# Performance work log

Hardware: AMD Instinct MI355X
Metric: run time of the kernel (lower is better)

Reference implementation:

```python
import jax, jax.numpy as jnp
import numpy as np

N_NODES = 100000
N_EDGES = 1600000
HIDDEN = 128
STEPS = 4
N_GRAPHS = 64


def setup_inputs() -> dict:
    key = jax.random.key(0)
    ks = jax.random.split(key, 8)
    x = jax.random.normal(ks[0], (N_NODES, HIDDEN), dtype=jnp.float32)
    edge_index = jax.random.randint(ks[1], (2, N_EDGES), 0, N_NODES, dtype=jnp.int64)
    batch = jnp.sort(jax.random.randint(ks[2], (N_NODES,), 0, N_GRAPHS, dtype=jnp.int64))
    s = 1.0 / np.sqrt(HIDDEN)
    weight = jax.random.normal(ks[3], (STEPS, HIDDEN, HIDDEN), dtype=jnp.float32) * s
    w_ih = jax.random.normal(ks[4], (3 * HIDDEN, HIDDEN), dtype=jnp.float32) * s
    w_hh = jax.random.normal(ks[5], (3 * HIDDEN, HIDDEN), dtype=jnp.float32) * s
    b_ih = jnp.zeros((3 * HIDDEN,), dtype=jnp.float32)
    b_hh = jnp.zeros((3 * HIDDEN,), dtype=jnp.float32)
    return {"x": x, "edge_index": edge_index, "batch": batch,
            "weight": weight, "w_ih": w_ih, "w_hh": w_hh,
            "b_ih": b_ih, "b_hh": b_hh}


def _gru_cell(m, h, w_ih, w_hh, b_ih, b_hh):
    # PyTorch GRUCell: gates ordered (r, z, n)
    gi = m @ w_ih.T + b_ih  # [N, 3H]
    gh = h @ w_hh.T + b_hh  # [N, 3H]
    i_r, i_z, i_n = jnp.split(gi, 3, axis=-1)
    h_r, h_z, h_n = jnp.split(gh, 3, axis=-1)
    r = jax.nn.sigmoid(i_r + h_r)
    z = jax.nn.sigmoid(i_z + h_z)
    n = jnp.tanh(i_n + r * h_n)
    return (1.0 - z) * n + z * h


def reference(x, edge_index, batch, weight, w_ih, w_hh, b_ih, b_hh):
    src, dst = edge_index[0], edge_index[1]
    h = x
    for i in range(STEPS):
        m = h @ weight[i]  # [N, H]
        # message = m[src] scattered (add) into dst
        aggr = jax.ops.segment_sum(m[src], dst, num_segments=N_NODES)
        h = _gru_cell(aggr, h, w_ih, w_hh, b_ih, b_hh)
    h = jax.nn.relu(h)
    # global mean pool per graph
    sums = jax.ops.segment_sum(h, batch, num_segments=N_GRAPHS)  # [G, H]
    counts = jax.ops.segment_sum(jnp.ones((N_NODES,), h.dtype), batch, num_segments=N_GRAPHS)
    return sums / jnp.maximum(counts, 1.0)[:, None]
```

## Files before the change

### kernel.cpp

```cpp
#include <hip/hip_runtime.h>

#define N_NODES  100000
#define N_EDGES  1600000
#define HIDDEN   128
#define STEPS    4
#define N_GRAPHS 64
#define NBUCK    256
#define BWID     391
#define BCAP     7168

typedef unsigned short u16;
typedef unsigned int   u32;
typedef unsigned long long u64;
typedef __attribute__((ext_vector_type(8))) short bf16x8;
typedef __attribute__((ext_vector_type(4))) float f32x4;
typedef __attribute__((ext_vector_type(2))) float f32x2;

__device__ inline u16 f2bf(float f) {
  u32 u = __float_as_uint(f);
  u = (u + 0x7FFFu + ((u >> 16) & 1u)) >> 16;
  return (u16)u;
}
__device__ inline float bf2f(u16 b) { return __uint_as_float(((u32)b) << 16); }

__device__ inline float rcp_f(float x) { return __builtin_amdgcn_rcpf(x); }
__device__ inline float sig_f(float x) { return rcp_f(1.f + __expf(-x)); }
__device__ inline float tanh_f(float x) { return 1.f - 2.f * rcp_f(1.f + __expf(2.f * x)); }

__global__ __launch_bounds__(1024) void k_part(const int* __restrict__ esrc,
                                               const int* __restrict__ edst,
                                               int* __restrict__ gcursor,
                                               u32* __restrict__ ebuf) {
  __shared__ int hist[NBUCK];
  __shared__ int base[NBUCK];
  int tid = threadIdx.x;
  if (tid < NBUCK) hist[tid] = 0;
  __syncthreads();
  int e0 = blockIdx.x * 4096;
  int sv[4], dv[4], bk[4], rk[4];
  #pragma unroll
  for (int i = 0; i < 4; ++i) {
    int e = e0 + i * 1024 + tid;
    if (e < N_EDGES) {
      sv[i] = esrc[e];
      dv[i] = edst[e];
      bk[i] = (int)((u32)dv[i] / (u32)BWID);
      rk[i] = atomicAdd(&hist[bk[i]], 1);
    } else bk[i] = -1;
  }
  __syncthreads();
  if (tid < NBUCK) base[tid] = atomicAdd(&gcursor[tid], hist[tid]);
  __syncthreads();
  #pragma unroll
  for (int i = 0; i < 4; ++i) {
    if (bk[i] >= 0) {
      int pos = bk[i] * BCAP + base[bk[i]] + rk[i];
      ebuf[pos] = ((u32)(dv[i] - bk[i] * BWID) << 17) | (u32)sv[i];
    }
  }
}

__global__ void k_bscan(const int* __restrict__ gcursor, int* __restrict__ ebase) {
  __shared__ int buf[NBUCK];
  int t = threadIdx.x;
  int v = gcursor[t];
  buf[t] = v;
  __syncthreads();
  for (int off = 1; off < NBUCK; off <<= 1) {
    int u = 0;
    if (t >= off) u = buf[t - off];
    __syncthreads();
    buf[t] += u;
    __syncthreads();
  }
  ebase[t] = buf[t] - v;
  if (t == NBUCK - 1) ebase[NBUCK] = buf[t];
}

__global__ __launch_bounds__(1024) void k_csr(const u32* __restrict__ ebuf,
                                              const int* __restrict__ ebase,
                                              int* __restrict__ offs,
                                              int* __restrict__ csr) {
  __shared__ int lcnt[512];
  __shared__ int lofs[512];
  int b = blockIdx.x, tid = threadIdx.x;
  int n0 = b * BWID;
  int n1 = min(n0 + BWID, N_NODES);
  int nn = n1 - n0;
  int e0 = ebase[b];
  int cnt = ebase[b + 1] - e0;
  const u32* ebase_p = ebuf + (size_t)b * BCAP;
  if (tid < 512) lcnt[tid] = 0;
  __syncthreads();
  for (int e = tid; e < cnt; e += 1024) {
    int dst = (int)(ebase_p[e] >> 17);
    atomicAdd(&lcnt[dst], 1);
  }
  __syncthreads();
  if (tid < 512) lofs[tid] = lcnt[tid];
  __syncthreads();
  for (int off = 1; off < 512; off <<= 1) {
    int v = 0;
    if (tid < 512 && tid >= off) v = lofs[tid - off];
    __syncthreads();
    if (tid < 512 && tid >= off) lofs[tid] += v;
    __syncthreads();
  }
  int nodeoff = 0;
  if (tid < 512) nodeoff = e0 + lofs[tid] - lcnt[tid];
  if (tid < 512) lofs[tid] = nodeoff;
  if (tid < nn) offs[n0 + tid] = nodeoff;
  if (b == 0 && tid == 0) offs[N_NODES] = N_EDGES;
  __syncthreads();
  for (int e = tid; e < cnt; e += 1024) {
    u32 p = ebase_p[e];
    int src = (int)(p & 0x1FFFFu);
    int dst = (int)(p >> 17);
    int pos = atomicAdd(&lofs[dst], 1);
    csr[pos] = src;
  }
}

__global__ void k_wb(const float* __restrict__ W, const float* __restrict__ w_ih,
                     const float* __restrict__ w_hh, u16* __restrict__ bsw) {
  __shared__ float wrow[128];
  int b = blockIdx.x, st = b >> 8, k = b & 255, t = threadIdx.x;
  if (k < 128) wrow[t] = W[(st * 128 + k) * 128 + t];
  __syncthreads();
  int kc = k >> 5, quad = (k >> 3) & 3, kl = k & 7;
  u16* base = bsw + (size_t)st * 131072 + kc * 16384;
  #pragma unroll
  for (int gq = 0; gq < 4; ++gq) {
    int c = gq * 128 + t;
    float v;
    if (k < 128) {
      if (c < 384) {
        const float* wr = w_ih + c * 128;
        float sacc = 0.f;
        for (int j = 0; j < 128; ++j) sacc += wrow[j] * wr[j];
        v = sacc;
      } else v = 0.f;
    } else {
      int kk = k - 128;
      if (c < 256)      v = w_hh[c * 128 + kk];
      else if (c < 384) v = 0.f;
      else              v = w_hh[(c - 128) * 128 + kk];
    }
    int gi = c >> 7, cw = c & 127;
    int wv = cw >> 5, hu = (cw >> 4) & 1, nl = c & 15;
    int slot = wv * 8 + gi * 2 + hu;
    base[(slot * 4 + quad) * 128 + nl * 8 + kl] = f2bf(v);
  }
}

__global__ void k_convert(const float* __restrict__ x, u16* __restrict__ h) {
  int i = (blockIdx.x * 256 + threadIdx.x) * 4;
  float4 v = *(const float4*)(x + i);
  u16 o[4] = {f2bf(v.x), f2bf(v.y), f2bf(v.z), f2bf(v.w)};
  *(uint2*)(h + i) = *(uint2*)o;
}

__device__ inline void acc8(f32x2* a, uint4 p) {
  f32x2 v;
  v.x = __uint_as_float(p.x << 16); v.y = __uint_as_float(p.x & 0xffff0000u);
  a[0] += v;
  v.x = __uint_as_float(p.y << 16); v.y = __uint_as_float(p.y & 0xffff0000u);
  a[1] += v;
  v.x = __uint_as_float(p.z << 16); v.y = __uint_as_float(p.z & 0xffff0000u);
  a[2] += v;
  v.x = __uint_as_float(p.w << 16); v.y = __uint_as_float(p.w & 0xffff0000u);
  a[3] += v;
}

__global__ void k_gather(const u16* __restrict__ h, const int* __restrict__ csr,
                         const int* __restrict__ offs, u16* __restrict__ s) {
  int node = blockIdx.x * 4 + (threadIdx.x >> 6);
  int lane = threadIdx.x & 63;
  int q   = lane >> 4;
  int sub = lane & 15;
  int beg = offs[node], end = offs[node + 1];
  f32x2 a[4];
  a[0] = a[1] = a[2] = a[3] = (f32x2){0.f, 0.f};
  int j = beg + q;
  for (; j + 12 < end; j += 16) {
    int s0 = csr[j], s1 = csr[j + 4], s2 = csr[j + 8], s3 = csr[j + 12];
    uint4 p0 = *(const uint4*)(h + (size_t)s0 * 128 + sub * 8);
    uint4 p1 = *(const uint4*)(h + (size_t)s1 * 128 + sub * 8);
    uint4 p2 = *(const uint4*)(h + (size_t)s2 * 128 + sub * 8);
    uint4 p3 = *(const uint4*)(h + (size_t)s3 * 128 + sub * 8);
    acc8(a, p0); acc8(a, p1); acc8(a, p2); acc8(a, p3);
  }
  {
    int j0 = j, j1 = j + 4, j2 = j + 8, j3 = j + 12;
    u32 m0 = (j0 < end) ? 0xffffffffu : 0u;
    u32 m1 = (j1 < end) ? 0xffffffffu : 0u;
    u32 m2 = (j2 < end) ? 0xffffffffu : 0u;
    u32 m3 = (j3 < end) ? 0xffffffffu : 0u;
    int t0 = (j0 < end) ? j0 : 0, t1 = (j1 < end) ? j1 : 0;
    int t2 = (j2 < end) ? j2 : 0, t3 = (j3 < end) ? j3 : 0;
    int s0 = csr[t0], s1 = csr[t1], s2 = csr[t2], s3 = csr[t3];
    uint4 p0 = *(const uint4*)(h + (size_t)s0 * 128 + sub * 8);
    uint4 p1 = *(const uint4*)(h + (size_t)s1 * 128 + sub * 8);
    uint4 p2 = *(const uint4*)(h + (size_t)s2 * 128 + sub * 8);
    uint4 p3 = *(const uint4*)(h + (size_t)s3 * 128 + sub * 8);
    p0.x &= m0; p0.y &= m0; p0.z &= m0; p0.w &= m0;
    p1.x &= m1; p1.y &= m1; p1.z &= m1; p1.w &= m1;
    p2.x &= m2; p2.y &= m2; p2.z &= m2; p2.w &= m2;
    p3.x &= m3; p3.y &= m3; p3.z &= m3; p3.w &= m3;
    acc8(a, p0); acc8(a, p1); acc8(a, p2); acc8(a, p3);
  }
  #pragma unroll
  for (int i = 0; i < 4; ++i) {
    a[i].x += __shfl_xor(a[i].x, 16); a[i].x += __shfl_xor(a[i].x, 32);
    a[i].y += __shfl_xor(a[i].y, 16); a[i].y += __shfl_xor(a[i].y, 32);
  }
  if (q == 0) {
    uint4 o;
    o.x = (u32)f2bf(a[0].x) | ((u32)f2bf(a[0].y) << 16);
    o.y = (u32)f2bf(a[1].x) | ((u32)f2bf(a[1].y) << 16);
    o.z = (u32)f2bf(a[2].x) | ((u32)f2bf(a[2].y) << 16);
    o.w = (u32)f2bf(a[3].x) | ((u32)f2bf(a[3].y) << 16);
    *(uint4*)(s + (size_t)node * 128 + sub * 8) = o;
  }
}

__global__ __launch_bounds__(256, 2) void k_gemm_gru(
    const u16* __restrict__ s_mat, const u16* __restrict__ h_mat,
    const u16* __restrict__ bsw, const float* __restrict__ b_ih,
    const float* __restrict__ b_hh, u16* __restrict__ h_out) {
  __shared__ u16 Asw[8192];

  const int tid  = threadIdx.x;
  const int wave = tid >> 6;
  const int lane = tid & 63;
  const int nl   = lane & 15;
  const int quad = lane >> 4;
  const int row0 = blockIdx.x * 32;

  {
    int snl = tid & 15, squad = (tid >> 4) & 3, sel = tid >> 6;
    int g = sel & 1, half = sel >> 1;
    const u16* row = (half ? h_mat : s_mat) + (size_t)(row0 + g * 16 + snl) * 128;
    #pragma unroll
    for (int kc2 = 0; kc2 < 4; ++kc2) {
      uint4 v = *(const uint4*)(row + kc2 * 32 + squad * 8);
      *(uint4*)&Asw[(((g * 8 + half * 4 + kc2) * 4 + squad) * 16 + snl) * 8] = v;
    }
  }
  __syncthreads();

  const u16* bp = bsw + wave * 8 * 512 + lane * 8;

  f32x4 acc[2][8];
  #pragma unroll
  for (int g = 0; g < 2; ++g)
    #pragma unroll
    for (int u = 0; u < 8; ++u) acc[g][u] = (f32x4){0.f, 0.f, 0.f, 0.f};

  bf16x8 b0[6], b1[6], b2[6];
  #pragma unroll
  for (int i = 0; i < 6; ++i) b0[i] = *(const bf16x8*)(bp + i * 512);
  #pragma unroll
  for (int i = 0; i < 6; ++i) b1[i] = *(const bf16x8*)(bp + 16384 + i * 512);

  #pragma unroll
  for (int kc = 0; kc < 8; ++kc) {
    if (kc < 6) {
      #pragma unroll
      for (int i = 0; i < 6; ++i) {
        int us = (kc + 2 < 4) ? i : (i < 4 ? i : i + 2);
        b2[i] = *(const bf16x8*)(bp + (kc + 2) * 16384 + us * 512);
      }
    }
    bf16x8 a0 = *(const bf16x8*)&Asw[kc * 512 + lane * 8];
    bf16x8 a1 = *(const bf16x8*)&Asw[(8 + kc) * 512 + lane * 8];
    #pragma unroll
    for (int i = 0; i < 6; ++i) {
      int u = (kc < 4) ? i : (i < 4 ? i : i + 2);
      acc[0][u] = __builtin_amdgcn_mfma_f32_16x16x32_bf16(a0, b0[i], acc[0][u], 0, 0, 0);
      acc[1][u] = __builtin_amdgcn_mfma_f32_16x16x32_bf16(a1, b0[i], acc[1][u], 0, 0, 0);
    }
    #pragma unroll
    for (int i = 0; i < 6; ++i) { b0[i] = b1[i]; b1[i] = b2[i]; }
  }

  float bias[8];
  #pragma unroll
  for (int u = 0; u < 8; ++u) {
    int gi = u >> 1, hu = u & 1;
    int cw = wave * 32 + hu * 16 + nl;
    bias[u] = (gi == 0) ? b_ih[cw] + b_hh[cw]
            : (gi == 1) ? b_ih[128 + cw] + b_hh[128 + cw]
            : (gi == 2) ? b_ih[256 + cw]
                        : b_hh[256 + cw];
  }

  #pragma unroll
  for (int g = 0; g < 2; ++g) {
    #pragma unroll
    for (int hu = 0; hu < 2; ++hu) {
      int cw = wave * 32 + hu * 16 + nl;
      int hbase = ((g * 8 + 4 + wave) * 4 + ((hu * 2 + (nl >> 3)) & 3)) * 128 + (nl & 7);
      #pragma unroll
      for (int i = 0; i < 4; ++i) {
        int m = quad * 4 + i;
        float rv = sig_f(acc[g][0 + hu][i] + bias[0 + hu]);
        float zv = sig_f(acc[g][2 + hu][i] + bias[2 + hu]);
        float iv = acc[g][4 + hu][i] + bias[4 + hu];
        float hn = acc[g][6 + hu][i] + bias[6 + hu];
        float hv = bf2f(Asw[hbase + m * 8]);
        float n  = tanh_f(iv + rv * hn);
        float o  = n + zv * (hv - n);
        h_out[(size_t)(row0 + g * 16 + m) * 128 + cw] = f2bf(o);
      }
    }
  }
}

__global__ void k_pool_partial(const u16* __restrict__ h, const int* __restrict__ batch,
                               float* __restrict__ acc) {
  int t = threadIdx.x;
  int node0 = blockIdx.x * 125;
  int node1 = node0 + 125;
  int cur = batch[node0];
  float sum = 0.f;
  for (int r = node0; r < node1; ++r) {
    int g = batch[r];
    if (g != cur) {
      atomicAdd(&acc[cur * 128 + t], sum);
      sum = 0.f;
      cur = g;
    }
    sum += fmaxf(bf2f(h[(size_t)r * 128 + t]), 0.f);
  }
  atomicAdd(&acc[cur * 128 + t], sum);
}

__global__ void k_pool_div(const float* __restrict__ acc, const int* __restrict__ batch,
                           float* __restrict__ out) {
  __shared__ int se[2];
  int g = blockIdx.x, t = threadIdx.x;
  if (t < 2) {
    int target = g + t;
    int lo = 0, hi = N_NODES;
    while (lo < hi) { int mid = (lo + hi) >> 1; if (batch[mid] < target) lo = mid + 1; else hi = mid; }
    se[t] = lo;
  }
  __syncthreads();
  int cnt = se[1] - se[0];
  out[g * 128 + t] = acc[g * 128 + t] / (float)(cnt > 0 ? cnt : 1);
}

extern "C" void kernel_launch(void* const* d_in, const int* in_sizes, int n_in,
                              void* d_out, int out_size, void* d_ws, size_t ws_size,
                              hipStream_t stream) {
  const float* x     = (const float*)d_in[0];
  const int*   edges = (const int*)d_in[1];
  const int*   batch = (const int*)d_in[2];
  const float* W     = (const float*)d_in[3];
  const float* w_ih  = (const float*)d_in[4];
  const float* w_hh  = (const float*)d_in[5];
  const float* b_ih  = (const float*)d_in[6];
  const float* b_hh  = (const float*)d_in[7];
  float* out = (float*)d_out;

  char* w = (char*)d_ws;
  u16* buf0    = (u16*)(w);
  u16* buf1    = (u16*)(w + 25600000);
  u16* bsw     = (u16*)(w + 51200000);
  float* acc   = (float*)(w + 52300032);
  int* offs    = (int*)(w + 52710400);
  int* gcursor = (int*)(w + 53120768);
  int* ebase   = (int*)(w + 53123328);
  int* csr     = (int*)(w + 53531136);
  u32* ebuf    = (u32*)buf1;

  const int* esrc = edges;
  const int* edst = edges + N_EDGES;

  hipMemsetAsync(gcursor, 0, NBUCK * sizeof(int), stream);
  k_part<<<391, 1024, 0, stream>>>(esrc, edst, gcursor, ebuf);
  k_bscan<<<1, NBUCK, 0, stream>>>(gcursor, ebase);
  k_csr<<<NBUCK, 1024, 0, stream>>>(ebuf, ebase, offs, csr);
  k_wb<<<1024, 128, 0, stream>>>(W, w_ih, w_hh, bsw);
  k_convert<<<(N_NODES * HIDDEN) / 1024, 256, 0, stream>>>(x, buf0);
  hipMemsetAsync(acc, 0, N_GRAPHS * HIDDEN * sizeof(float), stream);

  u16* hcur = buf0;
  u16* hnxt = buf1;
  for (int st = 0; st < STEPS; ++st) {
    k_gather<<<N_NODES / 4, 256, 0, stream>>>(hcur, csr, offs, hnxt);
    k_gemm_gru<<<N_NODES / 32, 256, 0, stream>>>(hnxt, hcur, bsw + st * 131072,
                                                 b_ih, b_hh, hnxt);
    u16* tmp = hcur; hcur = hnxt; hnxt = tmp;
  }
  k_pool_partial<<<800, 128, 0, stream>>>(hcur, batch, acc);
  k_pool_div<<<N_GRAPHS, 128, 0, stream>>>(acc, batch, out);
}
```

Before: 587.5 us.

## Per-wave histograms in partition, zero-row padding in gather, fold memset into scan

The partition kernel now keeps one LDS histogram per wave to cut contention on shared atomics, and turns the per-wave counts into prefix offsets after a single global atomic per bucket. The gather tail replaces masking of loaded values with redirection to an appended all-zero padding row. Row addresses are now built from 32-bit shift-or offsets instead of 64-bit multiplies. The accumulator memset is folded into the scan kernel, removing one API call, and the workspace offsets are repacked to make room for the padding rows, at the cost of more LDS in the partition kernel.

```diff
diff --git a/kernel.cpp b/kernel.cpp
--- a/kernel.cpp
+++ b/kernel.cpp
@@ -31,10 +31,12 @@
                                                const int* __restrict__ edst,
                                                int* __restrict__ gcursor,
                                                u32* __restrict__ ebuf) {
-  __shared__ int hist[NBUCK];
-  __shared__ int base[NBUCK];
+  __shared__ int hist[16][NBUCK];
+  __shared__ int base[16][NBUCK];
   int tid = threadIdx.x;
-  if (tid < NBUCK) hist[tid] = 0;
+  int wv  = tid >> 6;
+  #pragma unroll
+  for (int i = 0; i < 4; ++i) ((int*)hist)[tid + i * 1024] = 0;
   __syncthreads();
   int e0 = blockIdx.x * 4096;
   int sv[4], dv[4], bk[4], rk[4];
@@ -45,22 +47,31 @@
       sv[i] = esrc[e];
       dv[i] = edst[e];
       bk[i] = (int)((u32)dv[i] / (u32)BWID);
-      rk[i] = atomicAdd(&hist[bk[i]], 1);
+      rk[i] = atomicAdd(&hist[wv][bk[i]], 1);
     } else bk[i] = -1;
   }
   __syncthreads();
-  if (tid < NBUCK) base[tid] = atomicAdd(&gcursor[tid], hist[tid]);
+  if (tid < NBUCK) {
+    int c[16];
+    int sum = 0;
+    #pragma unroll
+    for (int w = 0; w < 16; ++w) { c[w] = hist[w][tid]; sum += c[w]; }
+    int g = atomicAdd(&gcursor[tid], sum);
+    #pragma unroll
+    for (int w = 0; w < 16; ++w) { base[w][tid] = g; g += c[w]; }
+  }
   __syncthreads();
   #pragma unroll
   for (int i = 0; i < 4; ++i) {
     if (bk[i] >= 0) {
-      int pos = bk[i] * BCAP + base[bk[i]] + rk[i];
+      int pos = bk[i] * BCAP + base[wv][bk[i]] + rk[i];
       ebuf[pos] = ((u32)(dv[i] - bk[i] * BWID) << 17) | (u32)sv[i];
     }
   }
 }
 
-__global__ void k_bscan(const int* __restrict__ gcursor, int* __restrict__ ebase) {
+__global__ void k_bscan(const int* __restrict__ gcursor, int* __restrict__ ebase,
+                        float* __restrict__ acc) {
   __shared__ int buf[NBUCK];
   int t = threadIdx.x;
   int v = gcursor[t];
@@ -75,6 +86,7 @@
   }
   ebase[t] = buf[t] - v;
   if (t == NBUCK - 1) ebase[NBUCK] = buf[t];
+  for (int i = t; i < N_GRAPHS * HIDDEN; i += NBUCK) acc[i] = 0.f;
 }
 
 __global__ __launch_bounds__(1024) void k_csr(const u32* __restrict__ ebuf,
@@ -153,11 +165,17 @@
   }
 }
 
-__global__ void k_convert(const float* __restrict__ x, u16* __restrict__ h) {
+__global__ void k_convert(const float* __restrict__ x, u16* __restrict__ h0,
+                          u16* __restrict__ h1) {
   int i = (blockIdx.x * 256 + threadIdx.x) * 4;
   float4 v = *(const float4*)(x + i);
   u16 o[4] = {f2bf(v.x), f2bf(v.y), f2bf(v.z), f2bf(v.w)};
-  *(uint2*)(h + i) = *(uint2*)o;
+  *(uint2*)(h0 + i) = *(uint2*)o;
+  if (blockIdx.x == 0) {
+    int t = threadIdx.x;
+    if (t < 64)       ((u32*)(h0 + (size_t)N_NODES * 128))[t] = 0;
+    else if (t < 128) ((u32*)(h1 + (size_t)N_NODES * 128))[t - 64] = 0;
+  }
 }
 
 __device__ inline void acc8(f32x2* a, uint4 p) {
@@ -171,6 +189,9 @@
   v.x = __uint_as_float(p.w << 16); v.y = __uint_as_float(p.w & 0xffff0000u);
   a[3] += v;
 }
+__device__ inline uint4 ldrow(const char* hb, u32 off) {
+  return *(const uint4*)(hb + off);
+}
 
 __global__ void k_gather(const u16* __restrict__ h, const int* __restrict__ csr,
                          const int* __restrict__ offs, u16* __restrict__ s) {
@@ -178,35 +199,32 @@
   int lane = threadIdx.x & 63;
   int q   = lane >> 4;
   int sub = lane & 15;
+  const char* hb = (const char*)h;
+  u32 co = (u32)(sub * 16);
   int beg = offs[node], end = offs[node + 1];
   f32x2 a[4];
   a[0] = a[1] = a[2] = a[3] = (f32x2){0.f, 0.f};
   int j = beg + q;
   for (; j + 12 < end; j += 16) {
-    int s0 = csr[j], s1 = csr[j + 4], s2 = csr[j + 8], s3 = csr[j + 12];
-    uint4 p0 = *(const uint4*)(h + (size_t)s0 * 128 + sub * 8);
-    uint4 p1 = *(const uint4*)(h + (size_t)s1 * 128 + sub * 8);
-    uint4 p2 = *(const uint4*)(h + (size_t)s2 * 128 + sub * 8);
-    uint4 p3 = *(const uint4*)(h + (size_t)s3 * 128 + sub * 8);
+    u32 s0 = (u32)csr[j], s1 = (u32)csr[j + 4], s2 = (u32)csr[j + 8], s3 = (u32)csr[j + 12];
+    uint4 p0 = ldrow(hb, (s0 << 8) | co);
+    uint4 p1 = ldrow(hb, (s1 << 8) | co);
+    uint4 p2 = ldrow(hb, (s2 << 8) | co);
+    uint4 p3 = ldrow(hb, (s3 << 8) | co);
     acc8(a, p0); acc8(a, p1); acc8(a, p2); acc8(a, p3);
   }
   {
     int j0 = j, j1 = j + 4, j2 = j + 8, j3 = j + 12;
-    u32 m0 = (j0 < end) ? 0xffffffffu : 0u;
-    u32 m1 = (j1 < end) ? 0xffffffffu : 0u;
-    u32 m2 = (j2 < end) ? 0xffffffffu : 0u;
-    u32 m3 = (j3 < end) ? 0xffffffffu : 0u;
     int t0 = (j0 < end) ? j0 : 0, t1 = (j1 < end) ? j1 : 0;
     int t2 = (j2 < end) ? j2 : 0, t3 = (j3 < end) ? j3 : 0;
-    int s0 = csr[t0], s1 = csr[t1], s2 = csr[t2], s3 = csr[t3];
-    uint4 p0 = *(const uint4*)(h + (size_t)s0 * 128 + sub * 8);
-    uint4 p1 = *(const uint4*)(h + (size_t)s1 * 128 + sub * 8);
-    uint4 p2 = *(const uint4*)(h + (size_t)s2 * 128 + sub * 8);
-    uint4 p3 = *(const uint4*)(h + (size_t)s3 * 128 + sub * 8);
-    p0.x &= m0; p0.y &= m0; p0.z &= m0; p0.w &= m0;
-    p1.x &= m1; p1.y &= m1; p1.z &= m1; p1.w &= m1;
-    p2.x &= m2; p2.y &= m2; p2.z &= m2; p2.w &= m2;
-    p3.x &= m3; p3.y &= m3; p3.z &= m3; p3.w &= m3;
+    u32 s0 = (u32)csr[t0]; s0 = (j0 < end) ? s0 : (u32)N_NODES;
+    u32 s1 = (u32)csr[t1]; s1 = (j1 < end) ? s1 : (u32)N_NODES;
+    u32 s2 = (u32)csr[t2]; s2 = (j2 < end) ? s2 : (u32)N_NODES;
+    u32 s3 = (u32)csr[t3]; s3 = (j3 < end) ? s3 : (u32)N_NODES;
+    uint4 p0 = ldrow(hb, (s0 << 8) | co);
+    uint4 p1 = ldrow(hb, (s1 << 8) | co);
+    uint4 p2 = ldrow(hb, (s2 << 8) | co);
+    uint4 p3 = ldrow(hb, (s3 << 8) | co);
     acc8(a, p0); acc8(a, p1); acc8(a, p2); acc8(a, p3);
   }
   #pragma unroll
@@ -366,13 +384,13 @@
 
   char* w = (char*)d_ws;
   u16* buf0    = (u16*)(w);
-  u16* buf1    = (u16*)(w + 25600000);
-  u16* bsw     = (u16*)(w + 51200000);
-  float* acc   = (float*)(w + 52300032);
-  int* offs    = (int*)(w + 52710400);
-  int* gcursor = (int*)(w + 53120768);
-  int* ebase   = (int*)(w + 53123328);
-  int* csr     = (int*)(w + 53531136);
+  u16* buf1    = (u16*)(w + 25600256);
+  u16* bsw     = (u16*)(w + 51200512);
+  float* acc   = (float*)(w + 52249088);
+  int* offs    = (int*)(w + 52281856);
+  int* gcursor = (int*)(w + 52682240);
+  int* ebase   = (int*)(w + 52683264);
+  int* csr     = (int*)(w + 52684800);
   u32* ebuf    = (u32*)buf1;
 
   const int* esrc = edges;
@@ -380,11 +398,10 @@
 
   hipMemsetAsync(gcursor, 0, NBUCK * sizeof(int), stream);
   k_part<<<391, 1024, 0, stream>>>(esrc, edst, gcursor, ebuf);
-  k_bscan<<<1, NBUCK, 0, stream>>>(gcursor, ebase);
+  k_bscan<<<1, NBUCK, 0, stream>>>(gcursor, ebase, acc);
   k_csr<<<NBUCK, 1024, 0, stream>>>(ebuf, ebase, offs, csr);
   k_wb<<<1024, 128, 0, stream>>>(W, w_ih, w_hh, bsw);
-  k_convert<<<(N_NODES * HIDDEN) / 1024, 256, 0, stream>>>(x, buf0);
-  hipMemsetAsync(acc, 0, N_GRAPHS * HIDDEN * sizeof(float), stream);
+  k_convert<<<(N_NODES * HIDDEN) / 1024, 256, 0, stream>>>(x, buf0, buf1);
 
   u16* hcur = buf0;
   u16* hnxt = buf1;
```

Result: no change. 583.0 us (-0.8%).
